# Performance work log

Measured on AMD Instinct MI355X. Metric: run time of the kernel, lower is better.

The kernel has to match this reference:

```python
import jax, jax.numpy as jnp
import numpy as np

SHIFT = 1
EPS = 1e-5

def setup_inputs() -> dict:
    key = jax.random.key(0)
    k1, k2, k3, k4, k5, k6 = jax.random.split(key, 6)
    B, C, H, Wd = 64, 512, 28, 28
    Cout = 512
    return {
        "x": jax.random.normal(k1, (B, C, H, Wd), dtype=jnp.float32),
        "W": jax.random.normal(k2, (Cout, C), dtype=jnp.float32) * 0.05,
        "gamma": jax.random.uniform(k3, (Cout,), dtype=jnp.float32) + 0.5,
        "beta": jax.random.normal(k4, (Cout,), dtype=jnp.float32) * 0.1,
        "running_mean": jax.random.normal(k5, (Cout,), dtype=jnp.float32) * 0.1,
        "running_var": jax.random.uniform(k6, (Cout,), dtype=jnp.float32) + 0.5,
    }

def reference(x, W, gamma, beta, running_mean, running_var):
    # Group-wise spatial shift: split channels into 4 groups, roll each.
    Cg = x.shape[1] // 4
    x1 = jnp.roll(x[:, 0*Cg:1*Cg], -SHIFT, axis=2)  # up
    x2 = jnp.roll(x[:, 1*Cg:2*Cg],  SHIFT, axis=2)  # down
    x3 = jnp.roll(x[:, 2*Cg:3*Cg], -SHIFT, axis=3)  # left
    x4 = jnp.roll(x[:, 3*Cg:4*Cg],  SHIFT, axis=3)  # right
    shifted = jnp.concatenate([x1, x2, x3, x4], axis=1)  # [B,C,H,W]
    # 1x1 conv (no bias) == channel matmul
    y = jnp.einsum('bchw,oc->bohw', shifted, W)
    # BatchNorm (inference: running stats) folded to scale/shift, then ReLU
    scale = gamma * jax.lax.rsqrt(running_var + EPS)
    shift = beta - running_mean * scale
    y = y * scale[None, :, None, None] + shift[None, :, None, None]
    return jnp.maximum(y, 0.0)
```

## Files before the change

### kernel.cpp

```cpp
#include <hip/hip_runtime.h>
#include <hip/hip_bf16.h>

#define BN   64
#define CIN  512
#define COUT 512
#define HW   784
#define NT   128
#define MT   112
#define BK   64

typedef __attribute__((ext_vector_type(8))) short short8;
typedef __attribute__((ext_vector_type(4))) float f32x4;

__device__ __forceinline__ unsigned short f2bf(float f) {
    union { float f; unsigned int u; } v; v.f = f;
    unsigned int r = v.u + 0x7fffu + ((v.u >> 16) & 1u);
    return (unsigned short)(r >> 16);
}

__device__ __forceinline__ uint2 pack4(float a, float b, float c, float d) {
    uint2 r;
    r.x = (unsigned int)f2bf(a) | ((unsigned int)f2bf(b) << 16);
    r.y = (unsigned int)f2bf(c) | ((unsigned int)f2bf(d) << 16);
    return r;
}

__device__ __forceinline__ void gl_lds16(const unsigned short* g, unsigned short* l) {
    __builtin_amdgcn_global_load_lds(
        (const __attribute__((address_space(1))) unsigned int*)g,
        (__attribute__((address_space(3))) unsigned int*)l,
        16, 0, 0);
}

__global__ __launch_bounds__(256)
void p1_shift_cvt(const float* __restrict__ x, const float* __restrict__ W,
                  unsigned short* __restrict__ Wb, unsigned short* __restrict__ Xt)
{
    const int t = threadIdx.x;
    if (blockIdx.z == BN) {
        int wlin = blockIdx.x * 7 + blockIdx.y;
        for (int gi = wlin * 256 + t; gi < (COUT * CIN) / 8; gi += 56 * 256) {
            const float* p = W + (size_t)gi * 8;
            float4 a = *(const float4*)p;
            float4 c = *(const float4*)(p + 4);
            uint2 lo = pack4(a.x, a.y, a.z, a.w);
            uint2 hi = pack4(c.x, c.y, c.z, c.w);
            uint4 v; v.x = lo.x; v.y = lo.y; v.z = hi.x; v.w = hi.y;
            *(uint4*)(Wb + (size_t)gi * 8) = v;
        }
        return;
    }
    const int kk = blockIdx.x;
    const int mt = blockIdx.y;
    const int b  = blockIdx.z;
    const int g  = kk >> 1;
    const int c0 = kk * BK;
    const int hw_base = mt * MT;
    const float* xb = x + (size_t)b * CIN * HW;
    unsigned short* Xb = Xt + (size_t)(b * 8 + kk) * HW * BK;

    #pragma unroll
    for (int e0 = 0; e0 < 2; ++e0) {
        int e = t + e0 * 256;
        if (e < (BK / 4) * (MT / 4)) {
            int cq = e / 28;
            int mq = e - cq * 28;
            int hw = hw_base + mq * 4;
            const float* src = xb + (size_t)(c0 + cq * 4) * HW;
            float4 v0, v1, v2, v3;
            if (g < 2) {
                int shw = hw + (g == 0 ? 28 : HW - 28);
                if (shw >= HW) shw -= HW;
                v0 = *(const float4*)(src + 0 * HW + shw);
                v1 = *(const float4*)(src + 1 * HW + shw);
                v2 = *(const float4*)(src + 2 * HW + shw);
                v3 = *(const float4*)(src + 3 * HW + shw);
            } else {
                int h  = hw / 28;
                int w0 = hw - h * 28;
                int base = h * 28;
                #pragma unroll
                for (int j = 0; j < 4; ++j) {
                    const float* row = src + j * HW + base;
                    float4 a = *(const float4*)(row + w0);
                    float4 r;
                    if (g == 2) {
                        float ex = row[(w0 + 4 < 28) ? (w0 + 4) : 0];
                        r.x = a.y; r.y = a.z; r.z = a.w; r.w = ex;
                    } else {
                        float ex = row[(w0 == 0) ? 27 : (w0 - 1)];
                        r.x = ex; r.y = a.x; r.z = a.y; r.w = a.z;
                    }
                    if (j == 0) v0 = r; else if (j == 1) v1 = r;
                    else if (j == 2) v2 = r; else v3 = r;
                }
            }
            unsigned short* dst = Xb + (size_t)hw * BK + cq * 4;
            *(uint2*)(dst + 0 * BK) = pack4(v0.x, v1.x, v2.x, v3.x);
            *(uint2*)(dst + 1 * BK) = pack4(v0.y, v1.y, v2.y, v3.y);
            *(uint2*)(dst + 2 * BK) = pack4(v0.z, v1.z, v2.z, v3.z);
            *(uint2*)(dst + 3 * BK) = pack4(v0.w, v1.w, v2.w, v3.w);
        }
    }
}

__global__ __launch_bounds__(256)
void p2_gemm(const unsigned short* __restrict__ Wb, const unsigned short* __restrict__ Xt,
             const float* __restrict__ gamma, const float* __restrict__ beta,
             const float* __restrict__ rmean, const float* __restrict__ rvar,
             float* __restrict__ out)
{
    __shared__ unsigned short sW[NT * BK];
    __shared__ unsigned short sX[MT * BK];

    const int t  = threadIdx.x;
    const int ot = blockIdx.x;
    const int mt = blockIdx.y;
    const int b  = blockIdx.z;
    const int o_base  = ot * NT;
    const int hw_base = mt * MT;
    const int lane = t & 63;
    const int wv   = t >> 6;
    const int m16  = lane & 15;
    const int q    = lane >> 4;

    f32x4 acc[2][7];
    #pragma unroll
    for (int i = 0; i < 2; ++i)
        #pragma unroll
        for (int j = 0; j < 7; ++j)
            acc[i][j] = (f32x4){0.f, 0.f, 0.f, 0.f};

    #pragma unroll
    for (int kk = 0; kk < CIN / BK; ++kk) {
        const int k0 = kk * BK;
        const unsigned short* Wk = Wb + (size_t)o_base * CIN + k0;
        #pragma unroll
        for (int i = 0; i < 4; ++i) {
            int ci = wv * 4 + i;
            int ch = ci * 64 + lane;
            int ol = ch >> 3, sl = ch & 7;
            int cs = sl ^ (ol & 7);
            gl_lds16(Wk + (size_t)ol * CIN + cs * 8, &sW[ci * 512]);
        }
        const unsigned short* Xk = Xt + ((size_t)(b * 8 + kk) * HW + hw_base) * BK;
        int nci = (wv < 2) ? 4 : 3;
        for (int i = 0; i < nci; ++i) {
            int ci = wv + 4 * i;
            int ch = ci * 64 + lane;
            int hl = ch >> 3, sl = ch & 7;
            int cs = sl ^ (hl & 7);
            gl_lds16(Xk + hl * BK + cs * 8, &sX[ci * 512]);
        }
        __syncthreads();

        #pragma unroll
        for (int ks = 0; ks < BK; ks += 32) {
            const int csb = (ks >> 3) + q;
            short8 af[2];
            #pragma unroll
            for (int bo = 0; bo < 2; ++bo) {
                int ro = wv * 32 + bo * 16 + m16;
                af[bo] = *(const short8*)(&sW[ro * BK + (csb ^ (ro & 7)) * 8]);
            }
            #pragma unroll
            for (int bm = 0; bm < 7; ++bm) {
                int m = bm * 16 + m16;
                short8 bf = *(const short8*)(&sX[m * BK + (csb ^ (m & 7)) * 8]);
                acc[0][bm] = __builtin_amdgcn_mfma_f32_16x16x32_bf16(af[0], bf, acc[0][bm], 0, 0, 0);
                acc[1][bm] = __builtin_amdgcn_mfma_f32_16x16x32_bf16(af[1], bf, acc[1][bm], 0, 0, 0);
            }
        }
        __syncthreads();
    }

    float scl[2][4], shf[2][4];
    #pragma unroll
    for (int bo = 0; bo < 2; ++bo)
        #pragma unroll
        for (int r = 0; r < 4; ++r) {
            int o = o_base + wv * 32 + bo * 16 + q * 4 + r;
            float sc = gamma[o] * rsqrtf(rvar[o] + 1e-5f);
            scl[bo][r] = sc;
            shf[bo][r] = beta[o] - rmean[o] * sc;
        }
    float* outb = out + (size_t)b * COUT * HW;
    #pragma unroll
    for (int bo = 0; bo < 2; ++bo) {
        #pragma unroll
        for (int r = 0; r < 4; ++r) {
            int o = o_base + wv * 32 + bo * 16 + q * 4 + r;
            float* orow = outb + (size_t)o * HW + hw_base + m16;
            #pragma unroll
            for (int bm = 0; bm < 7; ++bm) {
                float y = acc[bo][bm][r] * scl[bo][r] + shf[bo][r];
                y = fmaxf(y, 0.f);
                __builtin_nontemporal_store(y, orow + bm * 16);
            }
        }
    }
}

#define SW_STRIDE 72
#define SX_STRIDE 64
__global__ __launch_bounds__(256, 2)
void shiftconv_fallback(const float* __restrict__ x, const float* __restrict__ Wf,
                        const float* __restrict__ gamma, const float* __restrict__ beta,
                        const float* __restrict__ rmean, const float* __restrict__ rvar,
                        float* __restrict__ out)
{
    __shared__ unsigned short sW[NT * SW_STRIDE];
    __shared__ unsigned short sX[MT * SX_STRIDE];
    const int t = threadIdx.x;
    const int ot = blockIdx.x, mt = blockIdx.y, b = blockIdx.z;
    const int o_base = ot * NT, hw_base = mt * MT;
    const float* xb = x + (size_t)b * CIN * HW;
    const int lane = t & 63, wv = t >> 6, m16 = lane & 15, q = lane >> 4;
    f32x4 acc[2][7];
    #pragma unroll
    for (int i = 0; i < 2; ++i)
        #pragma unroll
        for (int j = 0; j < 7; ++j) acc[i][j] = (f32x4){0.f, 0.f, 0.f, 0.f};
    #pragma unroll
    for (int kk = 0; kk < CIN / BK; ++kk) {
        const int k0 = kk * BK;
        const int g = k0 >> 7;
        #pragma unroll
        for (int e0 = 0; e0 < 2; ++e0) {
            int e = t + e0 * 256;
            if (e < (BK / 4) * (MT / 4)) {
                int cq = e / 28, mq = e - cq * 28;
                int hw = hw_base + mq * 4;
                const float* src = xb + (size_t)(k0 + cq * 4) * HW;
                float4 v0, v1, v2, v3;
                if (g < 2) {
                    int shw = hw + (g == 0 ? 28 : HW - 28);
                    if (shw >= HW) shw -= HW;
                    v0 = *(const float4*)(src + 0 * HW + shw);
                    v1 = *(const float4*)(src + 1 * HW + shw);
                    v2 = *(const float4*)(src + 2 * HW + shw);
                    v3 = *(const float4*)(src + 3 * HW + shw);
                } else {
                    int h = hw / 28, w0 = hw - h * 28, base = h * 28;
                    #pragma unroll
                    for (int j = 0; j < 4; ++j) {
                        const float* row = src + j * HW + base;
                        float4 a = *(const float4*)(row + w0);
                        float4 r;
                        if (g == 2) {
                            float ex = row[(w0 + 4 < 28) ? (w0 + 4) : 0];
                            r.x = a.y; r.y = a.z; r.z = a.w; r.w = ex;
                        } else {
                            float ex = row[(w0 == 0) ? 27 : (w0 - 1)];
                            r.x = ex; r.y = a.x; r.z = a.y; r.w = a.z;
                        }
                        if (j == 0) v0 = r; else if (j == 1) v1 = r;
                        else if (j == 2) v2 = r; else v3 = r;
                    }
                }
                int m0 = mq * 4;
                { int p = (cq + 5 * (m0 + 0)) & 15;
                  *(uint2*)(&sX[(m0 + 0) * SX_STRIDE + p * 4]) = pack4(v0.x, v1.x, v2.x, v3.x); }
                { int p = (cq + 5 * (m0 + 1)) & 15;
                  *(uint2*)(&sX[(m0 + 1) * SX_STRIDE + p * 4]) = pack4(v0.y, v1.y, v2.y, v3.y); }
                { int p = (cq + 5 * (m0 + 2)) & 15;
                  *(uint2*)(&sX[(m0 + 2) * SX_STRIDE + p * 4]) = pack4(v0.z, v1.z, v2.z, v3.z); }
                { int p = (cq + 5 * (m0 + 3)) & 15;
                  *(uint2*)(&sX[(m0 + 3) * SX_STRIDE + p * 4]) = pack4(v0.w, v1.w, v2.w, v3.w); }
            }
        }
        #pragma unroll
        for (int i = 0; i < 4; ++i) {
            int e = t + i * 256;
            int ol = e >> 3, kg = (e & 7) * 8;
            const float* wr = Wf + (size_t)(o_base + ol) * CIN + k0 + kg;
            float4 a = *(const float4*)(wr);
            float4 c = *(const float4*)(wr + 4);
            uint2 lo = pack4(a.x, a.y, a.z, a.w);
            uint2 hi = pack4(c.x, c.y, c.z, c.w);
            uint4 v; v.x = lo.x; v.y = lo.y; v.z = hi.x; v.w = hi.y;
            *(uint4*)(&sW[ol * SW_STRIDE + kg]) = v;
        }
        __syncthreads();
        #pragma unroll
        for (int ks = 0; ks < BK; ks += 32) {
            short8 afrag[2];
            #pragma unroll
            for (int bo = 0; bo < 2; ++bo) {
                int row = wv * 32 + bo * 16 + m16;
                afrag[bo] = *(const short8*)(&sW[row * SW_STRIDE + ks + q * 8]);
            }
            #pragma unroll
            for (int bm = 0; bm < 7; ++bm) {
                int m = bm * 16 + m16;
                int g0 = (ks >> 2) + 2 * q;
                int p0 = (g0 + 5 * m) & 15;
                int p1 = (g0 + 1 + 5 * m) & 15;
                uint2 lo = *(const uint2*)(&sX[m * SX_STRIDE + p0 * 4]);
                uint2 hi = *(const uint2*)(&sX[m * SX_STRIDE + p1 * 4]);
                union { uint2 u2[2]; short8 s; } fb;
                fb.u2[0] = lo; fb.u2[1] = hi;
                acc[0][bm] = __builtin_amdgcn_mfma_f32_16x16x32_bf16(afrag[0], fb.s, acc[0][bm], 0, 0, 0);
                acc[1][bm] = __builtin_amdgcn_mfma_f32_16x16x32_bf16(afrag[1], fb.s, acc[1][bm], 0, 0, 0);
            }
        }
        __syncthreads();
    }
    float scl[2][4], shf[2][4];
    #pragma unroll
    for (int bo = 0; bo < 2; ++bo)
        #pragma unroll
        for (int r = 0; r < 4; ++r) {
            int o = o_base + wv * 32 + bo * 16 + q * 4 + r;
            float sc = gamma[o] * rsqrtf(rvar[o] + 1e-5f);
            scl[bo][r] = sc;
            shf[bo][r] = beta[o] - rmean[o] * sc;
        }
    float* outb = out + (size_t)b * COUT * HW;
    #pragma unroll
    for (int bo = 0; bo < 2; ++bo)
        #pragma unroll
        for (int r = 0; r < 4; ++r) {
            int o = o_base + wv * 32 + bo * 16 + q * 4 + r;
            float* orow = outb + (size_t)o * HW + hw_base + m16;
            #pragma unroll
            for (int bm = 0; bm < 7; ++bm) {
                float y = acc[bo][bm][r] * scl[bo][r] + shf[bo][r];
                y = fmaxf(y, 0.f);
                __builtin_nontemporal_store(y, orow + bm * 16);
            }
        }
}

extern "C" void kernel_launch(void* const* d_in, const int* in_sizes, int n_in,
                              void* d_out, int out_size, void* d_ws, size_t ws_size,
                              hipStream_t stream)
{
    const float* x     = (const float*)d_in[0];
    const float* W     = (const float*)d_in[1];
    const float* gamma = (const float*)d_in[2];
    const float* beta  = (const float*)d_in[3];
    const float* rmean = (const float*)d_in[4];
    const float* rvar  = (const float*)d_in[5];
    float* out = (float*)d_out;

    const size_t wb_bytes = (size_t)COUT * CIN * 2;
    const size_t xt_bytes = (size_t)BN * CIN * HW * 2;
    if (ws_size >= wb_bytes + xt_bytes) {
        unsigned short* Wb = (unsigned short*)d_ws;
        unsigned short* Xt = (unsigned short*)((char*)d_ws + wb_bytes);
        dim3 g1(8, 7, BN + 1);
        p1_shift_cvt<<<g1, 256, 0, stream>>>(x, W, Wb, Xt);
        dim3 g2(COUT / NT, HW / MT, BN);
        p2_gemm<<<g2, 256, 0, stream>>>(Wb, Xt, gamma, beta, rmean, rvar, out);
    } else {
        dim3 grid(COUT / NT, HW / MT, BN);
        shiftconv_fallback<<<grid, 256, 0, stream>>>(x, W, gamma, beta, rmean, rvar, out);
    }
}
```

Before: 256.3 us.

## Double-buffer X tiles, keep W in registers, remap grid, coalesce transpose stores

The GEMM kernel now loads each wave's full weight slice for all of K into registers up front and drops the shared-memory W tile. X tiles are double-buffered so the load for the next K step is issued before the current one is computed. The grid is flattened to 1792 blocks with an index remap that groups blocks sharing the same batch and spatial tile, aiming for better L2 reuse, and launch bounds request two blocks per SM. The shift/convert kernel stages its transposed bf16 tile in padded shared memory and writes 16-byte coalesced rows instead of scattered 8-byte stores. Holding 32 short8 weight fragments costs a lot of VGPRs, which may limit occupancy or cause spills.

```diff
diff --git a/kernel.cpp b/kernel.cpp
--- a/kernel.cpp
+++ b/kernel.cpp
@@ -8,6 +8,7 @@
 #define NT   128
 #define MT   112
 #define BK   64
+#define TROW 68
 
 typedef __attribute__((ext_vector_type(8))) short short8;
 typedef __attribute__((ext_vector_type(4))) float f32x4;
@@ -36,6 +37,7 @@
 void p1_shift_cvt(const float* __restrict__ x, const float* __restrict__ W,
                   unsigned short* __restrict__ Wb, unsigned short* __restrict__ Xt)
 {
+    __shared__ unsigned short sT[MT * TROW];
     const int t = threadIdx.x;
     if (blockIdx.z == BN) {
         int wlin = blockIdx.x * 7 + blockIdx.y;
@@ -57,7 +59,6 @@
     const int c0 = kk * BK;
     const int hw_base = mt * MT;
     const float* xb = x + (size_t)b * CIN * HW;
-    unsigned short* Xb = Xt + (size_t)(b * 8 + kk) * HW * BK;
 
     #pragma unroll
     for (int e0 = 0; e0 < 2; ++e0) {
@@ -95,28 +96,39 @@
                     else if (j == 2) v2 = r; else v3 = r;
                 }
             }
-            unsigned short* dst = Xb + (size_t)hw * BK + cq * 4;
-            *(uint2*)(dst + 0 * BK) = pack4(v0.x, v1.x, v2.x, v3.x);
-            *(uint2*)(dst + 1 * BK) = pack4(v0.y, v1.y, v2.y, v3.y);
-            *(uint2*)(dst + 2 * BK) = pack4(v0.z, v1.z, v2.z, v3.z);
-            *(uint2*)(dst + 3 * BK) = pack4(v0.w, v1.w, v2.w, v3.w);
-        }
-    }
-}
-
-__global__ __launch_bounds__(256)
+            int m0 = mq * 4;
+            *(uint2*)(&sT[(m0 + 0) * TROW + cq * 4]) = pack4(v0.x, v1.x, v2.x, v3.x);
+            *(uint2*)(&sT[(m0 + 1) * TROW + cq * 4]) = pack4(v0.y, v1.y, v2.y, v3.y);
+            *(uint2*)(&sT[(m0 + 2) * TROW + cq * 4]) = pack4(v0.z, v1.z, v2.z, v3.z);
+            *(uint2*)(&sT[(m0 + 3) * TROW + cq * 4]) = pack4(v0.w, v1.w, v2.w, v3.w);
+        }
+    }
+    __syncthreads();
+
+    unsigned short* Xb = Xt + ((size_t)(b * 8 + kk) * HW + hw_base) * BK;
+    for (int ch = t; ch < MT * 8; ch += 256) {
+        int m = ch >> 3, j = ch & 7;
+        uint2 a = *(const uint2*)(&sT[m * TROW + j * 8]);
+        uint2 c = *(const uint2*)(&sT[m * TROW + j * 8 + 4]);
+        uint4 v; v.x = a.x; v.y = a.y; v.z = c.x; v.w = c.y;
+        *(uint4*)(Xb + (size_t)m * BK + j * 8) = v;
+    }
+}
+
+__global__ __launch_bounds__(256, 2)
 void p2_gemm(const unsigned short* __restrict__ Wb, const unsigned short* __restrict__ Xt,
              const float* __restrict__ gamma, const float* __restrict__ beta,
              const float* __restrict__ rmean, const float* __restrict__ rvar,
              float* __restrict__ out)
 {
-    __shared__ unsigned short sW[NT * BK];
-    __shared__ unsigned short sX[MT * BK];
+    __shared__ unsigned short sX[2][MT * BK];
 
     const int t  = threadIdx.x;
-    const int ot = blockIdx.x;
-    const int mt = blockIdx.y;
-    const int b  = blockIdx.z;
+    const int id   = blockIdx.x;
+    const int ot   = (id >> 3) & 3;
+    const int pair = ((id >> 5) << 3) | (id & 7);
+    const int mt   = pair % 7;
+    const int b    = pair / 7;
     const int o_base  = ot * NT;
     const int hw_base = mt * MT;
     const int lane = t & 63;
@@ -124,51 +136,58 @@
     const int m16  = lane & 15;
     const int q    = lane >> 4;
 
-    f32x4 acc[2][7];
-    #pragma unroll
-    for (int i = 0; i < 2; ++i)
-        #pragma unroll
-        for (int j = 0; j < 7; ++j)
-            acc[i][j] = (f32x4){0.f, 0.f, 0.f, 0.f};
-
-    #pragma unroll
-    for (int kk = 0; kk < CIN / BK; ++kk) {
-        const int k0 = kk * BK;
-        const unsigned short* Wk = Wb + (size_t)o_base * CIN + k0;
-        #pragma unroll
-        for (int i = 0; i < 4; ++i) {
-            int ci = wv * 4 + i;
-            int ch = ci * 64 + lane;
-            int ol = ch >> 3, sl = ch & 7;
-            int cs = sl ^ (ol & 7);
-            gl_lds16(Wk + (size_t)ol * CIN + cs * 8, &sW[ci * 512]);
-        }
-        const unsigned short* Xk = Xt + ((size_t)(b * 8 + kk) * HW + hw_base) * BK;
+    const unsigned short* Xbase = Xt + ((size_t)(b * 8) * HW + hw_base) * BK;
+
+    auto stage = [&](int kk, unsigned short* buf) {
+        const unsigned short* Xk = Xbase + (size_t)kk * HW * BK;
         int nci = (wv < 2) ? 4 : 3;
         for (int i = 0; i < nci; ++i) {
             int ci = wv + 4 * i;
             int ch = ci * 64 + lane;
             int hl = ch >> 3, sl = ch & 7;
             int cs = sl ^ (hl & 7);
-            gl_lds16(Xk + hl * BK + cs * 8, &sX[ci * 512]);
-        }
-        __syncthreads();
-
-        #pragma unroll
-        for (int ks = 0; ks < BK; ks += 32) {
-            const int csb = (ks >> 3) + q;
-            short8 af[2];
-            #pragma unroll
-            for (int bo = 0; bo < 2; ++bo) {
-                int ro = wv * 32 + bo * 16 + m16;
-                af[bo] = *(const short8*)(&sW[ro * BK + (csb ^ (ro & 7)) * 8]);
-            }
-            #pragma unroll
-            for (int bm = 0; bm < 7; ++bm) {
-                int m = bm * 16 + m16;
-                short8 bf = *(const short8*)(&sX[m * BK + (csb ^ (m & 7)) * 8]);
-                acc[0][bm] = __builtin_amdgcn_mfma_f32_16x16x32_bf16(af[0], bf, acc[0][bm], 0, 0, 0);
-                acc[1][bm] = __builtin_amdgcn_mfma_f32_16x16x32_bf16(af[1], bf, acc[1][bm], 0, 0, 0);
+            gl_lds16(Xk + hl * BK + cs * 8, &buf[ci * 512]);
+        }
+    };
+
+    stage(0, sX[0]);
+
+    short8 wf[16][2];
+    #pragma unroll
+    for (int ki = 0; ki < 16; ++ki)
+        #pragma unroll
+        for (int bo = 0; bo < 2; ++bo) {
+            int row = o_base + wv * 32 + bo * 16 + m16;
+            wf[ki][bo] = *(const short8*)(Wb + (size_t)row * CIN + ki * 32 + q * 8);
+        }
+
+    f32x4 acc[2][7];
+    #pragma unroll
+    for (int i = 0; i < 2; ++i)
+        #pragma unroll
+        for (int j = 0; j < 7; ++j)
+            acc[i][j] = (f32x4){0.f, 0.f, 0.f, 0.f};
+
+    __syncthreads();
+
+    #pragma unroll
+    for (int kk = 0; kk < CIN / BK; ++kk) {
+        if (kk < 7) stage(kk + 1, sX[(kk + 1) & 1]);
+        const unsigned short* xs = sX[kk & 1];
+        #pragma unroll
+        for (int ks = 0; ks < 2; ++ks) {
+            short8 bf[7];
+            #pragma unroll
+            for (int bm = 0; bm < 7; ++bm) {
+                int m  = bm * 16 + m16;
+                int lc = ks * 4 + q;
+                int sl = lc ^ (m & 7);
+                bf[bm] = *(const short8*)(&xs[m * BK + sl * 8]);
+            }
+            #pragma unroll
+            for (int bm = 0; bm < 7; ++bm) {
+                acc[0][bm] = __builtin_amdgcn_mfma_f32_16x16x32_bf16(wf[kk * 2 + ks][0], bf[bm], acc[0][bm], 0, 0, 0);
+                acc[1][bm] = __builtin_amdgcn_mfma_f32_16x16x32_bf16(wf[kk * 2 + ks][1], bf[bm], acc[1][bm], 0, 0, 0);
             }
         }
         __syncthreads();
@@ -351,8 +370,7 @@
         unsigned short* Xt = (unsigned short*)((char*)d_ws + wb_bytes);
         dim3 g1(8, 7, BN + 1);
         p1_shift_cvt<<<g1, 256, 0, stream>>>(x, W, Wb, Xt);
-        dim3 g2(COUT / NT, HW / MT, BN);
-        p2_gemm<<<g2, 256, 0, stream>>>(Wb, Xt, gamma, beta, rmean, rvar, out);
+        p2_gemm<<<1792, 256, 0, stream>>>(Wb, Xt, gamma, beta, rmean, rvar, out);
     } else {
         dim3 grid(COUT / NT, HW / MT, BN);
         shiftconv_fallback<<<grid, 256, 0, stream>>>(x, W, gamma, beta, rmean, rvar, out);
```

Measured after the change: 237.2 us. 1.08x faster.
